# Kernel optimization log

Measured on AMD Instinct MI355X. Metric: run time of the kernel, lower is better.

Reference implementation:

```python
import jax, jax.numpy as jnp
import numpy as np

TEMPERATURE = 0.07
EPS = 1e-12  # F.normalize eps


def setup_inputs() -> dict:
    key = jax.random.key(0)
    k1, k2 = jax.random.split(key)
    B, D = 4096, 1024
    return {
        "features_1": jax.random.normal(k1, (B, D), dtype=jnp.float32),
        "features_2": jax.random.normal(k2, (B, D), dtype=jnp.float32),
    }


def _l2_normalize(x):
    n = jnp.sqrt(jnp.sum(x * x, axis=1, keepdims=True))
    return x / jnp.maximum(n, EPS)


def reference(features_1, features_2):
    B = features_1.shape[0]
    f1 = _l2_normalize(features_1)
    f2 = _l2_normalize(features_2)
    f = jnp.concatenate([f1, f2], axis=0)  # [2B, D]
    # cosine sim of already-normalized vectors == plain matmul
    sim = (f @ f.T) / TEMPERATURE  # [2B, 2B]
    # denominator: logsumexp over each row excluding the diagonal (self-sim)
    eye = jnp.eye(2 * B, dtype=bool)
    lse = jax.nn.logsumexp(jnp.where(eye, -jnp.inf, sim), axis=1)  # [2B]
    # positives: cross-view pairs (i+B, i) then (i, i+B)
    idx = jnp.arange(B)
    pos = jnp.concatenate([sim[idx + B, idx], sim[idx, idx + B]], axis=0)  # [2B]
    loss = -jnp.mean(pos - lse)
    return loss
```

## Files before the change

### kernel.cpp

```cpp
#include <hip/hip_runtime.h>
#include <hip/hip_bf16.h>
#include <math.h>

#define INV_T (1.0f / 0.07f)

typedef __bf16 bf16x8 __attribute__((ext_vector_type(8)));
typedef float f32x4 __attribute__((ext_vector_type(4)));

__device__ __forceinline__ void gld16(const void* g, void* l) {
    __builtin_amdgcn_global_load_lds(
        (const __attribute__((address_space(1))) unsigned int*)g,
        (__attribute__((address_space(3))) unsigned int*)l,
        16, 0, 0);
}

__global__ __launch_bounds__(256) void norm_kernel(
    const float4* __restrict__ f1, const float4* __restrict__ f2,
    ushort4* __restrict__ F, float* __restrict__ S, float* __restrict__ P,
    int B) {
    const int i = blockIdx.x;
    const int t = threadIdx.x;

    float4 x = f1[i * 256 + t];
    float4 y = f2[i * 256 + t];

    float s1 = x.x * x.x + x.y * x.y + x.z * x.z + x.w * x.w;
    float s2 = y.x * y.x + y.y * y.y + y.z * y.z + y.w * y.w;
    float dd = x.x * y.x + x.y * y.y + x.z * y.z + x.w * y.w;

    for (int o = 32; o > 0; o >>= 1) {
        s1 += __shfl_down(s1, o);
        s2 += __shfl_down(s2, o);
        dd += __shfl_down(dd, o);
    }
    __shared__ float red[4][3];
    const int wv = t >> 6, ln = t & 63;
    if (ln == 0) { red[wv][0] = s1; red[wv][1] = s2; red[wv][2] = dd; }
    __syncthreads();
    s1 = red[0][0] + red[1][0] + red[2][0] + red[3][0];
    s2 = red[0][1] + red[1][1] + red[2][1] + red[3][1];
    dd = red[0][2] + red[1][2] + red[2][2] + red[3][2];

    const float rn1 = 1.0f / fmaxf(sqrtf(s1), 1e-12f);
    const float rn2 = 1.0f / fmaxf(sqrtf(s2), 1e-12f);

    union { ushort4 u; __hip_bfloat16 h[4]; } p;
    p.h[0] = __float2bfloat16(x.x * rn1);
    p.h[1] = __float2bfloat16(x.y * rn1);
    p.h[2] = __float2bfloat16(x.z * rn1);
    p.h[3] = __float2bfloat16(x.w * rn1);
    F[(size_t)i * 256 + t] = p.u;
    p.h[0] = __float2bfloat16(y.x * rn2);
    p.h[1] = __float2bfloat16(y.y * rn2);
    p.h[2] = __float2bfloat16(y.z * rn2);
    p.h[3] = __float2bfloat16(y.w * rn2);
    F[(size_t)(B + i) * 256 + t] = p.u;

    if (t == 0) {
        P[i] = dd * rn1 * rn2;
        S[i] = 0.0f;
        S[B + i] = 0.0f;
    }
}

__global__ __launch_bounds__(256, 2) void sim_kernel(
    const __hip_bfloat16* __restrict__ F, float* __restrict__ S,
    int N, int D) {
    __shared__ __align__(16) __hip_bfloat16 As[128][64];
    __shared__ __align__(16) __hip_bfloat16 Bs[256][64];

    const int k = blockIdx.x;
    int tj = (int)((sqrtf(4.0f * (float)k + 1.0f) - 1.0f) * 0.5f);
    while ((tj + 1) * (tj + 2) <= k) ++tj;
    while (tj * (tj + 1) > k) --tj;
    const int ti = k - tj * (tj + 1);
    const int bRow = ti * 128;
    const int bCol = tj * 256;

    const int tid  = threadIdx.x;
    const int wave = tid >> 6;
    const int lane = tid & 63;
    const int quad = lane >> 4;
    const int l16  = lane & 15;

    const int srow   = lane >> 3;
    const int ldsOff = (lane & 7) * 8;
    const int srcOff = ((lane & 7) ^ srow) * 8;

    const int waveRow = (wave >> 1) * 64;
    const int waveCol = (wave & 1) * 128;
    const int swz = l16 & 7;

    f32x4 acc[4][8];
#pragma unroll
    for (int mi = 0; mi < 4; ++mi)
#pragma unroll
        for (int ni = 0; ni < 8; ++ni)
            acc[mi][ni] = (f32x4){0.0f, 0.0f, 0.0f, 0.0f};

    for (int kb = 0; kb < D; kb += 64) {
#pragma unroll
        for (int p = 0; p < 4; ++p) {
            const int rowT = (p * 4 + wave) * 8 + srow;
            gld16(&F[(size_t)(bRow + rowT) * D + kb + srcOff], &As[rowT][ldsOff]);
        }
#pragma unroll
        for (int p = 0; p < 8; ++p) {
            const int rowT = (p * 4 + wave) * 8 + srow;
            gld16(&F[(size_t)(bCol + rowT) * D + kb + srcOff], &Bs[rowT][ldsOff]);
        }
        __syncthreads();

#pragma unroll
        for (int ks = 0; ks < 2; ++ks) {
            const int slot = ((ks * 4 + quad) ^ swz) * 8;
            bf16x8 bf[8];
#pragma unroll
            for (int ni = 0; ni < 8; ++ni)
                bf[ni] = *(const bf16x8*)&Bs[waveCol + ni * 16 + l16][slot];
#pragma unroll
            for (int mi = 0; mi < 4; ++mi) {
                const bf16x8 af = *(const bf16x8*)&As[waveRow + mi * 16 + l16][slot];
#pragma unroll
                for (int ni = 0; ni < 8; ++ni)
                    acc[mi][ni] = __builtin_amdgcn_mfma_f32_16x16x32_bf16(
                        af, bf[ni], acc[mi][ni], 0, 0, 0);
            }
        }
        __syncthreads();
    }

#pragma unroll
    for (int mi = 0; mi < 4; ++mi)
#pragma unroll
        for (int ni = 0; ni < 8; ++ni)
#pragma unroll
            for (int r = 0; r < 4; ++r) {
                const int gRow = bRow + waveRow + mi * 16 + quad * 4 + r;
                const int gCol = bCol + waveCol + ni * 16 + l16;
                acc[mi][ni][r] = (gRow < gCol)
                    ? __expf((acc[mi][ni][r] - 1.0f) * INV_T) : 0.0f;
            }

#pragma unroll
    for (int mi = 0; mi < 4; ++mi)
#pragma unroll
        for (int r = 0; r < 4; ++r) {
            const int gRow = bRow + waveRow + mi * 16 + quad * 4 + r;
            float v = 0.0f;
#pragma unroll
            for (int ni = 0; ni < 8; ++ni) v += acc[mi][ni][r];
            v += __shfl_xor(v, 1);
            v += __shfl_xor(v, 2);
            v += __shfl_xor(v, 4);
            v += __shfl_xor(v, 8);
            if (l16 == 0) atomicAdd(&S[gRow], v);
        }

#pragma unroll
    for (int ni = 0; ni < 8; ++ni) {
        float cv = 0.0f;
#pragma unroll
        for (int mi = 0; mi < 4; ++mi)
#pragma unroll
            for (int r = 0; r < 4; ++r) cv += acc[mi][ni][r];
        cv += __shfl_xor(cv, 16);
        cv += __shfl_xor(cv, 32);
        if (quad == 0) atomicAdd(&S[bCol + waveCol + ni * 16 + l16], cv);
    }
}

__global__ __launch_bounds__(256) void finalize_kernel(
    const float* __restrict__ S, const float* __restrict__ P,
    float* __restrict__ out, int N, int B) {
    float s = 0.0f;
    for (int i = threadIdx.x; i < N; i += 256) s += __logf(S[i]);
    float pp = 0.0f;
    for (int i = threadIdx.x; i < B; i += 256) pp += P[i];
    for (int o = 32; o > 0; o >>= 1) {
        s += __shfl_down(s, o);
        pp += __shfl_down(pp, o);
    }
    __shared__ float red[4][2];
    if ((threadIdx.x & 63) == 0) {
        red[threadIdx.x >> 6][0] = s;
        red[threadIdx.x >> 6][1] = pp;
    }
    __syncthreads();
    if (threadIdx.x == 0) {
        const float sl = red[0][0] + red[1][0] + red[2][0] + red[3][0];
        const float ps = red[0][1] + red[1][1] + red[2][1] + red[3][1];
        out[0] = INV_T + sl / (float)N - ps * (2.0f * INV_T / (float)N);
    }
}

extern "C" void kernel_launch(void* const* d_in, const int* in_sizes, int n_in,
                              void* d_out, int out_size, void* d_ws, size_t ws_size,
                              hipStream_t stream) {
    const int D = 1024;
    const int B = in_sizes[0] / D;
    const int N = 2 * B;
    const int M2 = N / 256;
    const int ntiles = M2 * M2 + M2;

    const float* f1 = (const float*)d_in[0];
    const float* f2 = (const float*)d_in[1];

    __hip_bfloat16* F = (__hip_bfloat16*)d_ws;
    float* S = (float*)((char*)d_ws + (size_t)N * D * sizeof(__hip_bfloat16));
    float* P = S + N;

    norm_kernel<<<dim3(B), dim3(256), 0, stream>>>(
        (const float4*)f1, (const float4*)f2, (ushort4*)F, S, P, B);
    sim_kernel<<<dim3(ntiles), dim3(256), 0, stream>>>(F, S, N, D);
    finalize_kernel<<<dim3(1), dim3(256), 0, stream>>>(S, P, (float*)d_out, N, B);
}
```

Measured before the change: 179.4 us.

## Load B operand directly to registers, double-buffer A tile, fuse finalize via ticket

The B tile is no longer staged through LDS; each lane reads its bf16x8 fragments straight from global memory, while the A tile is double-buffered in LDS with the next chunk prefetched during compute. The separate finalize kernel is removed: the last sim block, found with an atomic ticket counter reset in norm_kernel, does the final log-sum reduction. This cuts LDS traffic and one kernel launch, but the direct global B loads are uncoalesced 16-byte reads that may stall the MFMA loop.

```diff
diff --git a/kernel.cpp b/kernel.cpp
--- a/kernel.cpp
+++ b/kernel.cpp
@@ -17,7 +17,7 @@
 __global__ __launch_bounds__(256) void norm_kernel(
     const float4* __restrict__ f1, const float4* __restrict__ f2,
     ushort4* __restrict__ F, float* __restrict__ S, float* __restrict__ P,
-    int B) {
+    unsigned int* __restrict__ cnt, int B) {
     const int i = blockIdx.x;
     const int t = threadIdx.x;
 
@@ -60,14 +60,15 @@
         P[i] = dd * rn1 * rn2;
         S[i] = 0.0f;
         S[B + i] = 0.0f;
+        if (i == 0) *cnt = 0u;
     }
 }
 
 __global__ __launch_bounds__(256, 2) void sim_kernel(
     const __hip_bfloat16* __restrict__ F, float* __restrict__ S,
-    int N, int D) {
-    __shared__ __align__(16) __hip_bfloat16 As[128][64];
-    __shared__ __align__(16) __hip_bfloat16 Bs[256][64];
+    const float* __restrict__ P, unsigned int* __restrict__ cnt,
+    float* __restrict__ out, int N, int D, int B) {
+    __shared__ __align__(16) __hip_bfloat16 As[2][128][64];
 
     const int k = blockIdx.x;
     int tj = (int)((sqrtf(4.0f * (float)k + 1.0f) - 1.0f) * 0.5f);
@@ -91,6 +92,8 @@
     const int waveCol = (wave & 1) * 128;
     const int swz = l16 & 7;
 
+    const __hip_bfloat16* bp = F + (size_t)(bCol + waveCol + l16) * D + quad * 8;
+
     f32x4 acc[4][8];
 #pragma unroll
     for (int mi = 0; mi < 4; ++mi)
@@ -98,33 +101,39 @@
         for (int ni = 0; ni < 8; ++ni)
             acc[mi][ni] = (f32x4){0.0f, 0.0f, 0.0f, 0.0f};
 
-    for (int kb = 0; kb < D; kb += 64) {
-#pragma unroll
-        for (int p = 0; p < 4; ++p) {
-            const int rowT = (p * 4 + wave) * 8 + srow;
-            gld16(&F[(size_t)(bRow + rowT) * D + kb + srcOff], &As[rowT][ldsOff]);
-        }
-#pragma unroll
-        for (int p = 0; p < 8; ++p) {
-            const int rowT = (p * 4 + wave) * 8 + srow;
-            gld16(&F[(size_t)(bCol + rowT) * D + kb + srcOff], &Bs[rowT][ldsOff]);
-        }
-        __syncthreads();
-
+#pragma unroll
+    for (int p = 0; p < 4; ++p) {
+        const int rowT = (p * 4 + wave) * 8 + srow;
+        gld16(&F[(size_t)(bRow + rowT) * D + srcOff], &As[0][rowT][ldsOff]);
+    }
+    __syncthreads();
+
+    const int NIT = D / 64;
+    for (int it = 0; it < NIT; ++it) {
+        const int kb = it * 64;
+        if (it + 1 < NIT) {
+#pragma unroll
+            for (int p = 0; p < 4; ++p) {
+                const int rowT = (p * 4 + wave) * 8 + srow;
+                gld16(&F[(size_t)(bRow + rowT) * D + kb + 64 + srcOff],
+                      &As[(it + 1) & 1][rowT][ldsOff]);
+            }
+        }
+        const int buf = it & 1;
 #pragma unroll
         for (int ks = 0; ks < 2; ++ks) {
             const int slot = ((ks * 4 + quad) ^ swz) * 8;
-            bf16x8 bf[8];
+            bf16x8 bfr[8];
 #pragma unroll
             for (int ni = 0; ni < 8; ++ni)
-                bf[ni] = *(const bf16x8*)&Bs[waveCol + ni * 16 + l16][slot];
+                bfr[ni] = *(const bf16x8*)(bp + (size_t)ni * 16 * D + kb + ks * 32);
 #pragma unroll
             for (int mi = 0; mi < 4; ++mi) {
-                const bf16x8 af = *(const bf16x8*)&As[waveRow + mi * 16 + l16][slot];
+                const bf16x8 af = *(const bf16x8*)&As[buf][waveRow + mi * 16 + l16][slot];
 #pragma unroll
                 for (int ni = 0; ni < 8; ++ni)
                     acc[mi][ni] = __builtin_amdgcn_mfma_f32_16x16x32_bf16(
-                        af, bf[ni], acc[mi][ni], 0, 0, 0);
+                        af, bfr[ni], acc[mi][ni], 0, 0, 0);
             }
         }
         __syncthreads();
@@ -168,29 +177,30 @@
         cv += __shfl_xor(cv, 32);
         if (quad == 0) atomicAdd(&S[bCol + waveCol + ni * 16 + l16], cv);
     }
-}
-
-__global__ __launch_bounds__(256) void finalize_kernel(
-    const float* __restrict__ S, const float* __restrict__ P,
-    float* __restrict__ out, int N, int B) {
-    float s = 0.0f;
-    for (int i = threadIdx.x; i < N; i += 256) s += __logf(S[i]);
-    float pp = 0.0f;
-    for (int i = threadIdx.x; i < B; i += 256) pp += P[i];
-    for (int o = 32; o > 0; o >>= 1) {
-        s += __shfl_down(s, o);
-        pp += __shfl_down(pp, o);
-    }
-    __shared__ float red[4][2];
-    if ((threadIdx.x & 63) == 0) {
-        red[threadIdx.x >> 6][0] = s;
-        red[threadIdx.x >> 6][1] = pp;
-    }
+
+    __threadfence();
+    __shared__ unsigned int ticket;
+    if (tid == 0) ticket = atomicAdd(cnt, 1u);
     __syncthreads();
-    if (threadIdx.x == 0) {
-        const float sl = red[0][0] + red[1][0] + red[2][0] + red[3][0];
-        const float ps = red[0][1] + red[1][1] + red[2][1] + red[3][1];
-        out[0] = INV_T + sl / (float)N - ps * (2.0f * INV_T / (float)N);
+    if (ticket == (unsigned int)(gridDim.x - 1)) {
+        __threadfence();
+        volatile const float* Sv = S;
+        float s = 0.0f;
+        for (int i = tid; i < N; i += 256) s += __logf(Sv[i]);
+        float pp = 0.0f;
+        for (int i = tid; i < B; i += 256) pp += P[i];
+        for (int o = 32; o > 0; o >>= 1) {
+            s += __shfl_down(s, o);
+            pp += __shfl_down(pp, o);
+        }
+        __shared__ float red[4][2];
+        if ((tid & 63) == 0) { red[tid >> 6][0] = s; red[tid >> 6][1] = pp; }
+        __syncthreads();
+        if (tid == 0) {
+            const float sl = red[0][0] + red[1][0] + red[2][0] + red[3][0];
+            const float ps = red[0][1] + red[1][1] + red[2][1] + red[3][1];
+            out[0] = INV_T + sl / (float)N - ps * (2.0f * INV_T / (float)N);
+        }
     }
 }
 
@@ -209,9 +219,10 @@
     __hip_bfloat16* F = (__hip_bfloat16*)d_ws;
     float* S = (float*)((char*)d_ws + (size_t)N * D * sizeof(__hip_bfloat16));
     float* P = S + N;
+    unsigned int* cnt = (unsigned int*)(P + B);
 
     norm_kernel<<<dim3(B), dim3(256), 0, stream>>>(
-        (const float4*)f1, (const float4*)f2, (ushort4*)F, S, P, B);
-    sim_kernel<<<dim3(ntiles), dim3(256), 0, stream>>>(F, S, N, D);
-    finalize_kernel<<<dim3(1), dim3(256), 0, stream>>>(S, P, (float*)d_out, N, B);
-}
+        (const float4*)f1, (const float4*)f2, (ushort4*)F, S, P, cnt, B);
+    sim_kernel<<<dim3(ntiles), dim3(256), 0, stream>>>(
+        F, S, P, cnt, (float*)d_out, N, D, B);
+}
```

Measured after the change: 319.8 us. 78.3% more time.
